# Kernel tuning notes

Hardware: AMD Instinct MI355X
Metric: run time of the kernel (lower is better)

## Reference

```python
import jax, jax.numpy as jnp
import numpy as np

STATE_DIM = 2
HIDDEN = 1024
N_SKILLS = 5
N_ACTIONS = 4
BATCH = 65536


def setup_inputs() -> dict:
    key = jax.random.key(0)
    ks = jax.random.split(key, 8)
    def lin_init(k, fan_in, shape):
        bound = 1.0 / np.sqrt(fan_in)
        return jax.random.uniform(k, shape, jnp.float32, -bound, bound)
    return {
        "s": jax.random.normal(ks[0], (BATCH, STATE_DIM), jnp.float32),
        "skill_idx": jax.random.randint(ks[1], (BATCH,), 0, N_SKILLS, jnp.int32),
        "W1": lin_init(ks[2], STATE_DIM, (STATE_DIM, HIDDEN)),
        "b1": lin_init(ks[3], STATE_DIM, (HIDDEN,)),
        "W2": lin_init(ks[4], HIDDEN, (HIDDEN, HIDDEN)),
        "b2": lin_init(ks[5], HIDDEN, (HIDDEN,)),
        "W_heads": lin_init(ks[6], HIDDEN, (N_SKILLS, HIDDEN, N_ACTIONS)),
        "b_heads": lin_init(ks[7], HIDDEN, (N_SKILLS, N_ACTIONS)),
    }


def reference(s, skill_idx, W1, b1, W2, b2, W_heads, b_heads):
    # shared feature MLP: Linear -> ReLU -> Linear -> ReLU
    h = jax.nn.relu(s @ W1 + b1)            # [B, H]
    feat = jax.nn.relu(h @ W2 + b2)         # [B, H]
    # per-sample skill head: gather weights then one batched contraction
    Wg = W_heads[skill_idx]                 # [B, H, A]
    bg = b_heads[skill_idx]                 # [B, A]
    return jnp.einsum('bh,bha->ba', feat, Wg) + bg  # [B, A]
```

## Files before the change

### kernel.cpp

```cpp
#include <hip/hip_runtime.h>

typedef __bf16 bf16x8 __attribute__((ext_vector_type(8)));
typedef __bf16 bf16x4 __attribute__((ext_vector_type(4)));
typedef float  floatx4 __attribute__((ext_vector_type(4)));

#define GLOBAL_AS __attribute__((address_space(1)))
#define LOCAL_AS  __attribute__((address_space(3)))

static constexpr int HID = 1024;
static constexpr int MT  = 128;
static constexpr int BK  = 64;
static constexpr int KIT = HID / BK;

__device__ __forceinline__ void h8(bf16x8& d, float s0, float s1,
                                   const float4& w0a, const float4& w0b,
                                   const float4& w1a, const float4& w1b,
                                   const float4& ba,  const float4& bb) {
    d[0] = (__bf16)fmaxf(fmaf(s1, w1a.x, fmaf(s0, w0a.x, ba.x)), 0.f);
    d[1] = (__bf16)fmaxf(fmaf(s1, w1a.y, fmaf(s0, w0a.y, ba.y)), 0.f);
    d[2] = (__bf16)fmaxf(fmaf(s1, w1a.z, fmaf(s0, w0a.z, ba.z)), 0.f);
    d[3] = (__bf16)fmaxf(fmaf(s1, w1a.w, fmaf(s0, w0a.w, ba.w)), 0.f);
    d[4] = (__bf16)fmaxf(fmaf(s1, w1b.x, fmaf(s0, w0b.x, bb.x)), 0.f);
    d[5] = (__bf16)fmaxf(fmaf(s1, w1b.y, fmaf(s0, w0b.y, bb.y)), 0.f);
    d[6] = (__bf16)fmaxf(fmaf(s1, w1b.z, fmaf(s0, w0b.z, bb.z)), 0.f);
    d[7] = (__bf16)fmaxf(fmaf(s1, w1b.w, fmaf(s0, w0b.w, bb.w)), 0.f);
}

__global__ __launch_bounds__(256)
void prep_all(const float* __restrict__ S,  const float* __restrict__ W1,
              const float* __restrict__ B1, const float* __restrict__ W2,
              const float* __restrict__ WH,
              __bf16* __restrict__ H, __bf16* __restrict__ W2T,
              __bf16* __restrict__ WHT, float* __restrict__ OUT,
              int row0, int nh, int nz) {
    if (blockIdx.x < (unsigned)nh) {
        const int wid  = blockIdx.x * 4 + (threadIdx.x >> 6);
        const int lane = threadIdx.x & 63;
        const int rb   = wid * 8;
        const int c0   = lane * 8;
        const float4 w0a0 = *(const float4*)(W1 + c0);
        const float4 w0b0 = *(const float4*)(W1 + c0 + 4);
        const float4 w1a0 = *(const float4*)(W1 + HID + c0);
        const float4 w1b0 = *(const float4*)(W1 + HID + c0 + 4);
        const float4 ba0  = *(const float4*)(B1 + c0);
        const float4 bb0  = *(const float4*)(B1 + c0 + 4);
        const float4 w0a1 = *(const float4*)(W1 + 512 + c0);
        const float4 w0b1 = *(const float4*)(W1 + 512 + c0 + 4);
        const float4 w1a1 = *(const float4*)(W1 + HID + 512 + c0);
        const float4 w1b1 = *(const float4*)(W1 + HID + 512 + c0 + 4);
        const float4 ba1  = *(const float4*)(B1 + 512 + c0);
        const float4 bb1  = *(const float4*)(B1 + 512 + c0 + 4);
        float2 sv[8];
#pragma unroll
        for (int r = 0; r < 8; ++r)
            sv[r] = *(const float2*)(S + (size_t)(row0 + rb + r) * 2);
#pragma unroll
        for (int r = 0; r < 8; ++r) {
            const int rl = rb + r;
            const int xo = ((((c0 >> 3) & 7) ^ (rl & 7)) << 3);
            bf16x8 hv0, hv1;
            h8(hv0, sv[r].x, sv[r].y, w0a0, w0b0, w1a0, w1b0, ba0, bb0);
            h8(hv1, sv[r].x, sv[r].y, w0a1, w0b1, w1a1, w1b1, ba1, bb1);
            *(bf16x8*)(H + (size_t)rl * HID + ((c0 & ~63) | xo))       = hv0;
            *(bf16x8*)(H + (size_t)rl * HID + ((c0 & ~63) | xo) + 512) = hv1;
        }
        return;
    }
    int b = blockIdx.x - nh;
    if (b < nz) {
        ((float4*)OUT)[(size_t)row0 + (size_t)b * 256 + threadIdx.x]
            = make_float4(0.f, 0.f, 0.f, 0.f);
        return;
    }
    b -= nz;
    if (b < 256) {
        __shared__ __bf16 tile[64][65];
        const int bx = b & 15;
        const int by = b >> 4;
        const int a  = threadIdx.x & 63;
        const int bb = threadIdx.x >> 6;
#pragma unroll
        for (int r = 0; r < 16; ++r) {
            const int k = r * 4 + bb;
            tile[a][k] = (__bf16)W2[(size_t)(by * 64 + k) * HID + bx * 64 + a];
        }
        __syncthreads();
#pragma unroll
        for (int r = 0; r < 16; ++r) {
            const int n = r * 4 + bb;
            const int g = a >> 3, j = a & 7;
            const int ksw = ((g ^ (n & 7)) << 3) | j;
            W2T[(size_t)(bx * 64 + n) * HID + by * 64 + ksw] = tile[n][a];
        }
    } else {
        const int r = b - 256;
        const int s = r >> 2, a = r & 3;
        for (int k = threadIdx.x; k < HID; k += 256) {
            const float v = (r < 20) ? WH[((size_t)s * HID + k) * 4 + a] : 0.f;
            const int c = k >> 7, o = (k >> 3) & 15, j = k & 7;
            const int sw = (o & 8) | ((o & 7) ^ (r & 7));
            WHT[(size_t)r * HID + c * 128 + sw * 8 + j] = (__bf16)v;
        }
    }
}

__global__ __launch_bounds__(256, 4)
void policy_main(const __bf16* __restrict__ H, const int* __restrict__ SK,
                 const __bf16* __restrict__ W2T, const float* __restrict__ B2,
                 const __bf16* __restrict__ WHT, const float* __restrict__ BH,
                 float* __restrict__ OUT, int row0, int mg_bits) {
    __shared__ __align__(16) char smem[40960];
    __bf16* hA    = (__bf16*)smem;
    __bf16* Bt    = (__bf16*)(smem + 16384);
    __bf16* featL = (__bf16*)smem;
    __bf16* WHTL  = (__bf16*)(smem + 32768);

    const int tid  = threadIdx.x;
    const int lane = tid & 63;
    const int wv   = tid >> 6;
    const int wm   = wv & 1;
    const int wn   = wv >> 1;
    const int l15  = lane & 15;
    const int quad = lane >> 4;
    const int n8   = blockIdx.x >> mg_bits;
    const int i0l  = (blockIdx.x & ((1 << mg_bits) - 1)) * MT;

    floatx4 acc[4][4] = {};
    floatx4 hacc[2][2] = {};

#pragma unroll
    for (int c = 0; c < 2; ++c) {
        const int rb = c * 16 + wv * 4;
        const __bf16* gp = WHT + (size_t)(rb + (lane >> 4)) * HID
                         + n8 * 128 + (lane & 15) * 8;
        __builtin_amdgcn_global_load_lds((GLOBAL_AS void*)gp,
                                         (LOCAL_AS void*)(WHTL + rb * 128), 16, 0, 0);
    }

#pragma unroll 1
    for (int kt = 0; kt < KIT; ++kt) {
        __syncthreads();
#pragma unroll
        for (int c = 0; c < 4; ++c) {
            const int rb = c * 32 + wv * 8;
            const __bf16* gp = H + (size_t)(i0l + rb + (lane >> 3)) * HID
                             + kt * BK + (lane & 7) * 8;
            __builtin_amdgcn_global_load_lds((GLOBAL_AS void*)gp,
                                             (LOCAL_AS void*)(hA + rb * 64), 16, 0, 0);
        }
#pragma unroll
        for (int c = 0; c < 4; ++c) {
            const int rb = c * 32 + wv * 8;
            const __bf16* gp = W2T + (size_t)(n8 * 128 + rb + (lane >> 3)) * HID
                             + kt * BK + (lane & 7) * 8;
            __builtin_amdgcn_global_load_lds((GLOBAL_AS void*)gp,
                                             (LOCAL_AS void*)(Bt + rb * 64), 16, 0, 0);
        }
        __syncthreads();
#pragma unroll
        for (int ks = 0; ks < 2; ++ks) {
            bf16x8 wf[4], hf[4];
#pragma unroll
            for (int f = 0; f < 4; ++f) {
                const int row = wn * 64 + f * 16 + l15;
                wf[f] = *(const bf16x8*)(Bt + row * 64 + (((ks * 4 + quad) ^ (row & 7)) * 8));
            }
#pragma unroll
            for (int f = 0; f < 4; ++f) {
                const int smp = wm * 64 + f * 16 + l15;
                hf[f] = *(const bf16x8*)(hA + smp * 64 + (((ks * 4 + quad) ^ (smp & 7)) * 8));
            }
#pragma unroll
            for (int fn = 0; fn < 4; ++fn)
#pragma unroll
                for (int fm = 0; fm < 4; ++fm)
                    acc[fn][fm] = __builtin_amdgcn_mfma_f32_16x16x32_bf16(
                        wf[fn], hf[fm], acc[fn][fm], 0, 0, 0);
        }
    }

    __syncthreads();
#pragma unroll
    for (int fn = 0; fn < 4; ++fn) {
        const int fcb = wn * 64 + fn * 16 + quad * 4;
        const float4 b2v = *(const float4*)(B2 + n8 * 128 + fcb);
#pragma unroll
        for (int fm = 0; fm < 4; ++fm) {
            const int smp = wm * 64 + fm * 16 + l15;
            const floatx4 v = acc[fn][fm];
            bf16x4 p;
            p[0] = (__bf16)fmaxf(v[0] + b2v.x, 0.f);
            p[1] = (__bf16)fmaxf(v[1] + b2v.y, 0.f);
            p[2] = (__bf16)fmaxf(v[2] + b2v.z, 0.f);
            p[3] = (__bf16)fmaxf(v[3] + b2v.w, 0.f);
            *(bf16x4*)(featL + smp * 128 + (((fcb >> 3) ^ (smp & 15)) << 3) + (fcb & 7)) = p;
        }
    }
    __syncthreads();

#pragma unroll
    for (int f2 = 0; f2 < 2; ++f2) {
#pragma unroll
        for (int ks2 = 0; ks2 < 4; ++ks2) {
            const int row = wv * 32 + f2 * 16 + l15;
            const bf16x8 fa = *(const bf16x8*)(featL + row * 128
                                 + (((ks2 * 4 + quad) ^ (row & 15)) << 3));
#pragma unroll
            for (int t2 = 0; t2 < 2; ++t2) {
                const int r = t2 * 16 + l15;
                const int o = ks2 * 4 + quad;
                const int sw = (o & 8) | ((o & 7) ^ (r & 7));
                const bf16x8 wb = *(const bf16x8*)(WHTL + r * 128 + sw * 8);
                hacc[f2][t2] = __builtin_amdgcn_mfma_f32_16x16x32_bf16(
                    fa, wb, hacc[f2][t2], 0, 0, 0);
            }
        }
    }

#pragma unroll
    for (int f2 = 0; f2 < 2; ++f2)
#pragma unroll
        for (int j = 0; j < 4; ++j) {
            const int smp = wv * 32 + f2 * 16 + quad * 4 + j;
            const int sk  = SK[(size_t)row0 + i0l + smp];
#pragma unroll
            for (int t2 = 0; t2 < 2; ++t2) {
                const int hc = t2 * 16 + l15;
                const int d  = hc - sk * 4;
                if (d >= 0 && d < 4) {
                    float v = hacc[f2][t2][j];
                    if (n8 == 0) v += BH[hc];
                    atomicAdd(&OUT[(size_t)(row0 + i0l + smp) * 4 + d], v);
                }
            }
        }
}

extern "C" void kernel_launch(void* const* d_in, const int* in_sizes, int n_in,
                              void* d_out, int out_size, void* d_ws, size_t ws_size,
                              hipStream_t stream) {
    const float* S  = (const float*)d_in[0];
    const int*   SK = (const int*)d_in[1];
    const float* W1 = (const float*)d_in[2];
    const float* B1 = (const float*)d_in[3];
    const float* W2 = (const float*)d_in[4];
    const float* B2 = (const float*)d_in[5];
    const float* WH = (const float*)d_in[6];
    const float* BH = (const float*)d_in[7];

    char* ws = (char*)d_ws;
    __bf16* W2T = (__bf16*)ws;
    __bf16* WHT = (__bf16*)(ws + 2 * 1024 * 1024);
    __bf16* H   = (__bf16*)(ws + 2 * 1024 * 1024 + 65536);

    const size_t fixed = 2 * 1024 * 1024 + 65536;
    const size_t avail = ws_size > fixed ? ws_size - fixed : 0;
    int nc = 1;
    while (nc < 64 && (size_t)(65536 / nc) * HID * sizeof(__bf16) > avail) nc <<= 1;
    const int Mc = 65536 / nc;
    int mg_bits = 0;
    while ((1 << mg_bits) < Mc / MT) ++mg_bits;

    for (int c = 0; c < nc; ++c) {
        const int nh = Mc / 32;
        const int nz = Mc / 256;
        const int extra = (c == 0) ? 288 : 0;
        hipLaunchKernelGGL(prep_all, dim3(nh + nz + extra), dim3(256), 0, stream,
                           S, W1, B1, W2, WH, H, W2T, WHT, (float*)d_out,
                           c * Mc, nh, nz);
        hipLaunchKernelGGL(policy_main, dim3((Mc / MT) * 8), dim3(256), 0, stream,
                           H, SK, W2T, B2, WHT, BH, (float*)d_out, c * Mc, mg_bits);
    }
}
```

Measured before the change: 239.6 us.

## Fuse prep and GEMM kernels into one persistent cooperative kernel with grid sync

Merges the weight-transpose, hidden-layer computation and output-zeroing kernel with the main GEMM kernel into a single persistent cooperative kernel. A grid-wide barrier separates the two phases, and tiles are processed in a grid-stride loop sized from the occupancy query. This removes one kernel launch per chunk and the gap between the two launches. In exchange it adds grid-sync overhead, and the persistent loop may lose some latency hiding compared with a full oversubscribed grid.

```diff
diff --git a/kernel.cpp b/kernel.cpp
--- a/kernel.cpp
+++ b/kernel.cpp
@@ -1,4 +1,7 @@
 #include <hip/hip_runtime.h>
+#include <hip/hip_cooperative_groups.h>
+
+namespace cg = cooperative_groups;
 
 typedef __bf16 bf16x8 __attribute__((ext_vector_type(8)));
 typedef __bf16 bf16x4 __attribute__((ext_vector_type(4)));
@@ -26,18 +29,59 @@
     d[7] = (__bf16)fmaxf(fmaf(s1, w1b.w, fmaf(s0, w0b.w, bb.w)), 0.f);
 }
 
-__global__ __launch_bounds__(256)
-void prep_all(const float* __restrict__ S,  const float* __restrict__ W1,
-              const float* __restrict__ B1, const float* __restrict__ W2,
-              const float* __restrict__ WH,
-              __bf16* __restrict__ H, __bf16* __restrict__ W2T,
-              __bf16* __restrict__ WHT, float* __restrict__ OUT,
-              int row0, int nh, int nz) {
-    if (blockIdx.x < (unsigned)nh) {
-        const int wid  = blockIdx.x * 4 + (threadIdx.x >> 6);
-        const int lane = threadIdx.x & 63;
-        const int rb   = wid * 8;
-        const int c0   = lane * 8;
+__global__ __launch_bounds__(256, 4)
+void policy_mega(const float* __restrict__ S,  const int* __restrict__ SK,
+                 const float* __restrict__ W1, const float* __restrict__ B1,
+                 const float* __restrict__ W2, const float* __restrict__ B2,
+                 const float* __restrict__ WH, const float* __restrict__ BH,
+                 __bf16* __restrict__ H, __bf16* __restrict__ W2T,
+                 __bf16* __restrict__ WHT, float* __restrict__ OUT,
+                 int row0, int Mc, int mg_bits, int do_weights) {
+    __shared__ __align__(16) char smem[40960];
+    __bf16* hA    = (__bf16*)smem;
+    __bf16* Bt    = (__bf16*)(smem + 16384);
+    __bf16* featL = (__bf16*)smem;
+    __bf16* WHTL  = (__bf16*)(smem + 32768);
+
+    const int tid  = threadIdx.x;
+    const int lane = tid & 63;
+    const int wv   = tid >> 6;
+    const int l15  = lane & 15;
+    const int quad = lane >> 4;
+
+    if (do_weights) {
+        for (int wb = blockIdx.x; wb < 288; wb += gridDim.x) {
+            if (wb < 256) {
+                __bf16 (*tile)[65] = (__bf16 (*)[65])smem;
+                const int bx = wb & 15, by = wb >> 4;
+                const int a = tid & 63, b4 = tid >> 6;
+#pragma unroll
+                for (int r = 0; r < 16; ++r) {
+                    const int k = r * 4 + b4;
+                    tile[a][k] = (__bf16)W2[(size_t)(by * 64 + k) * HID + bx * 64 + a];
+                }
+                __syncthreads();
+#pragma unroll
+                for (int r = 0; r < 16; ++r) {
+                    const int n = r * 4 + b4;
+                    const int g = a >> 3, j = a & 7;
+                    W2T[(size_t)(bx * 64 + n) * HID + by * 64
+                        + (((g ^ (n & 7)) << 3) | j)] = tile[n][a];
+                }
+                __syncthreads();
+            } else {
+                const int r = wb - 256, s = r >> 2, ac = r & 3;
+                for (int k = tid; k < HID; k += 256) {
+                    const float v = (r < 20) ? WH[((size_t)s * HID + k) * 4 + ac] : 0.f;
+                    const int cc = k >> 7, o = (k >> 3) & 15, j = k & 7;
+                    WHT[(size_t)r * HID + cc * 128
+                        + ((o & 8) | ((o & 7) ^ (r & 7))) * 8 + j] = (__bf16)v;
+                }
+            }
+        }
+    }
+    {
+        const int c0 = lane * 8;
         const float4 w0a0 = *(const float4*)(W1 + c0);
         const float4 w0b0 = *(const float4*)(W1 + c0 + 4);
         const float4 w1a0 = *(const float4*)(W1 + HID + c0);
@@ -50,190 +94,156 @@
         const float4 w1b1 = *(const float4*)(W1 + HID + 512 + c0 + 4);
         const float4 ba1  = *(const float4*)(B1 + 512 + c0);
         const float4 bb1  = *(const float4*)(B1 + 512 + c0 + 4);
-        float2 sv[8];
-#pragma unroll
-        for (int r = 0; r < 8; ++r)
-            sv[r] = *(const float2*)(S + (size_t)(row0 + rb + r) * 2);
-#pragma unroll
-        for (int r = 0; r < 8; ++r) {
-            const int rl = rb + r;
-            const int xo = ((((c0 >> 3) & 7) ^ (rl & 7)) << 3);
-            bf16x8 hv0, hv1;
-            h8(hv0, sv[r].x, sv[r].y, w0a0, w0b0, w1a0, w1b0, ba0, bb0);
-            h8(hv1, sv[r].x, sv[r].y, w0a1, w0b1, w1a1, w1b1, ba1, bb1);
-            *(bf16x8*)(H + (size_t)rl * HID + ((c0 & ~63) | xo))       = hv0;
-            *(bf16x8*)(H + (size_t)rl * HID + ((c0 & ~63) | xo) + 512) = hv1;
-        }
-        return;
-    }
-    int b = blockIdx.x - nh;
-    if (b < nz) {
-        ((float4*)OUT)[(size_t)row0 + (size_t)b * 256 + threadIdx.x]
-            = make_float4(0.f, 0.f, 0.f, 0.f);
-        return;
-    }
-    b -= nz;
-    if (b < 256) {
-        __shared__ __bf16 tile[64][65];
-        const int bx = b & 15;
-        const int by = b >> 4;
-        const int a  = threadIdx.x & 63;
-        const int bb = threadIdx.x >> 6;
-#pragma unroll
-        for (int r = 0; r < 16; ++r) {
-            const int k = r * 4 + bb;
-            tile[a][k] = (__bf16)W2[(size_t)(by * 64 + k) * HID + bx * 64 + a];
-        }
+        const int nwav = gridDim.x * 4;
+#pragma unroll 1
+        for (int g = blockIdx.x * 4 + wv; g < (Mc >> 3); g += nwav) {
+            const int rb = g * 8;
+            float2 sv[8];
+#pragma unroll
+            for (int r = 0; r < 8; ++r)
+                sv[r] = *(const float2*)(S + (size_t)(row0 + rb + r) * 2);
+#pragma unroll
+            for (int r = 0; r < 8; ++r) {
+                const int rl = rb + r;
+                const int xo = ((((c0 >> 3) & 7) ^ (rl & 7)) << 3);
+                bf16x8 hv0, hv1;
+                h8(hv0, sv[r].x, sv[r].y, w0a0, w0b0, w1a0, w1b0, ba0, bb0);
+                h8(hv1, sv[r].x, sv[r].y, w0a1, w0b1, w1a1, w1b1, ba1, bb1);
+                *(bf16x8*)(H + (size_t)rl * HID + ((c0 & ~63) | xo))       = hv0;
+                *(bf16x8*)(H + (size_t)rl * HID + ((c0 & ~63) | xo) + 512) = hv1;
+            }
+        }
+    }
+    {
+        const int stride = gridDim.x * 256;
+        for (int i = blockIdx.x * 256 + tid; i < Mc; i += stride)
+            ((float4*)OUT)[(size_t)row0 + i] = make_float4(0.f, 0.f, 0.f, 0.f);
+    }
+
+    cg::this_grid().sync();
+
+    const int ntiles = (Mc / MT) * 8;
+#pragma unroll 1
+    for (int tt = blockIdx.x; tt < ntiles; tt += gridDim.x) {
+        const int n8  = tt >> mg_bits;
+        const int i0l = (tt & ((1 << mg_bits) - 1)) * MT;
+        const int wm  = wv & 1;
+        const int wn  = wv >> 1;
+
         __syncthreads();
 #pragma unroll
-        for (int r = 0; r < 16; ++r) {
-            const int n = r * 4 + bb;
-            const int g = a >> 3, j = a & 7;
-            const int ksw = ((g ^ (n & 7)) << 3) | j;
-            W2T[(size_t)(bx * 64 + n) * HID + by * 64 + ksw] = tile[n][a];
-        }
-    } else {
-        const int r = b - 256;
-        const int s = r >> 2, a = r & 3;
-        for (int k = threadIdx.x; k < HID; k += 256) {
-            const float v = (r < 20) ? WH[((size_t)s * HID + k) * 4 + a] : 0.f;
-            const int c = k >> 7, o = (k >> 3) & 15, j = k & 7;
-            const int sw = (o & 8) | ((o & 7) ^ (r & 7));
-            WHT[(size_t)r * HID + c * 128 + sw * 8 + j] = (__bf16)v;
-        }
-    }
-}
-
-__global__ __launch_bounds__(256, 4)
-void policy_main(const __bf16* __restrict__ H, const int* __restrict__ SK,
-                 const __bf16* __restrict__ W2T, const float* __restrict__ B2,
-                 const __bf16* __restrict__ WHT, const float* __restrict__ BH,
-                 float* __restrict__ OUT, int row0, int mg_bits) {
-    __shared__ __align__(16) char smem[40960];
-    __bf16* hA    = (__bf16*)smem;
-    __bf16* Bt    = (__bf16*)(smem + 16384);
-    __bf16* featL = (__bf16*)smem;
-    __bf16* WHTL  = (__bf16*)(smem + 32768);
-
-    const int tid  = threadIdx.x;
-    const int lane = tid & 63;
-    const int wv   = tid >> 6;
-    const int wm   = wv & 1;
-    const int wn   = wv >> 1;
-    const int l15  = lane & 15;
-    const int quad = lane >> 4;
-    const int n8   = blockIdx.x >> mg_bits;
-    const int i0l  = (blockIdx.x & ((1 << mg_bits) - 1)) * MT;
-
-    floatx4 acc[4][4] = {};
-    floatx4 hacc[2][2] = {};
-
-#pragma unroll
-    for (int c = 0; c < 2; ++c) {
-        const int rb = c * 16 + wv * 4;
-        const __bf16* gp = WHT + (size_t)(rb + (lane >> 4)) * HID
-                         + n8 * 128 + (lane & 15) * 8;
-        __builtin_amdgcn_global_load_lds((GLOBAL_AS void*)gp,
-                                         (LOCAL_AS void*)(WHTL + rb * 128), 16, 0, 0);
-    }
+        for (int c = 0; c < 2; ++c) {
+            const int rb = c * 16 + wv * 4;
+            const __bf16* gp = WHT + (size_t)(rb + (lane >> 4)) * HID
+                             + n8 * 128 + (lane & 15) * 8;
+            __builtin_amdgcn_global_load_lds((GLOBAL_AS void*)gp,
+                                             (LOCAL_AS void*)(WHTL + rb * 128), 16, 0, 0);
+        }
+
+        floatx4 acc[4][4] = {};
+        floatx4 hacc[2][2] = {};
 
 #pragma unroll 1
-    for (int kt = 0; kt < KIT; ++kt) {
+        for (int kt = 0; kt < KIT; ++kt) {
+            __syncthreads();
+#pragma unroll
+            for (int c = 0; c < 4; ++c) {
+                const int rb = c * 32 + wv * 8;
+                const __bf16* gp = H + (size_t)(i0l + rb + (lane >> 3)) * HID
+                                 + kt * BK + (lane & 7) * 8;
+                __builtin_amdgcn_global_load_lds((GLOBAL_AS void*)gp,
+                                                 (LOCAL_AS void*)(hA + rb * 64), 16, 0, 0);
+            }
+#pragma unroll
+            for (int c = 0; c < 4; ++c) {
+                const int rb = c * 32 + wv * 8;
+                const __bf16* gp = W2T + (size_t)(n8 * 128 + rb + (lane >> 3)) * HID
+                                 + kt * BK + (lane & 7) * 8;
+                __builtin_amdgcn_global_load_lds((GLOBAL_AS void*)gp,
+                                                 (LOCAL_AS void*)(Bt + rb * 64), 16, 0, 0);
+            }
+            __syncthreads();
+#pragma unroll
+            for (int ks = 0; ks < 2; ++ks) {
+                bf16x8 wf[4], hf[4];
+#pragma unroll
+                for (int f = 0; f < 4; ++f) {
+                    const int row = wn * 64 + f * 16 + l15;
+                    wf[f] = *(const bf16x8*)(Bt + row * 64
+                                             + (((ks * 4 + quad) ^ (row & 7)) * 8));
+                }
+#pragma unroll
+                for (int f = 0; f < 4; ++f) {
+                    const int smp = wm * 64 + f * 16 + l15;
+                    hf[f] = *(const bf16x8*)(hA + smp * 64
+                                             + (((ks * 4 + quad) ^ (smp & 7)) * 8));
+                }
+#pragma unroll
+                for (int fn = 0; fn < 4; ++fn)
+#pragma unroll
+                    for (int fm = 0; fm < 4; ++fm)
+                        acc[fn][fm] = __builtin_amdgcn_mfma_f32_16x16x32_bf16(
+                            wf[fn], hf[fm], acc[fn][fm], 0, 0, 0);
+            }
+        }
+
         __syncthreads();
 #pragma unroll
-        for (int c = 0; c < 4; ++c) {
-            const int rb = c * 32 + wv * 8;
-            const __bf16* gp = H + (size_t)(i0l + rb + (lane >> 3)) * HID
-                             + kt * BK + (lane & 7) * 8;
-            __builtin_amdgcn_global_load_lds((GLOBAL_AS void*)gp,
-                                             (LOCAL_AS void*)(hA + rb * 64), 16, 0, 0);
-        }
-#pragma unroll
-        for (int c = 0; c < 4; ++c) {
-            const int rb = c * 32 + wv * 8;
-            const __bf16* gp = W2T + (size_t)(n8 * 128 + rb + (lane >> 3)) * HID
-                             + kt * BK + (lane & 7) * 8;
-            __builtin_amdgcn_global_load_lds((GLOBAL_AS void*)gp,
-                                             (LOCAL_AS void*)(Bt + rb * 64), 16, 0, 0);
+        for (int fn = 0; fn < 4; ++fn) {
+            const int fcb = wn * 64 + fn * 16 + quad * 4;
+            const float4 b2v = *(const float4*)(B2 + n8 * 128 + fcb);
+#pragma unroll
+            for (int fm = 0; fm < 4; ++fm) {
+                const int smp = wm * 64 + fm * 16 + l15;
+                const floatx4 v = acc[fn][fm];
+                bf16x4 p;
+                p[0] = (__bf16)fmaxf(v[0] + b2v.x, 0.f);
+                p[1] = (__bf16)fmaxf(v[1] + b2v.y, 0.f);
+                p[2] = (__bf16)fmaxf(v[2] + b2v.z, 0.f);
+                p[3] = (__bf16)fmaxf(v[3] + b2v.w, 0.f);
+                *(bf16x4*)(featL + smp * 128
+                           + (((fcb >> 3) ^ (smp & 15)) << 3) + (fcb & 7)) = p;
+            }
         }
         __syncthreads();
-#pragma unroll
-        for (int ks = 0; ks < 2; ++ks) {
-            bf16x8 wf[4], hf[4];
-#pragma unroll
-            for (int f = 0; f < 4; ++f) {
-                const int row = wn * 64 + f * 16 + l15;
-                wf[f] = *(const bf16x8*)(Bt + row * 64 + (((ks * 4 + quad) ^ (row & 7)) * 8));
-            }
-#pragma unroll
-            for (int f = 0; f < 4; ++f) {
-                const int smp = wm * 64 + f * 16 + l15;
-                hf[f] = *(const bf16x8*)(hA + smp * 64 + (((ks * 4 + quad) ^ (smp & 7)) * 8));
-            }
-#pragma unroll
-            for (int fn = 0; fn < 4; ++fn)
-#pragma unroll
-                for (int fm = 0; fm < 4; ++fm)
-                    acc[fn][fm] = __builtin_amdgcn_mfma_f32_16x16x32_bf16(
-                        wf[fn], hf[fm], acc[fn][fm], 0, 0, 0);
-        }
-    }
-
-    __syncthreads();
-#pragma unroll
-    for (int fn = 0; fn < 4; ++fn) {
-        const int fcb = wn * 64 + fn * 16 + quad * 4;
-        const float4 b2v = *(const float4*)(B2 + n8 * 128 + fcb);
-#pragma unroll
-        for (int fm = 0; fm < 4; ++fm) {
-            const int smp = wm * 64 + fm * 16 + l15;
-            const floatx4 v = acc[fn][fm];
-            bf16x4 p;
-            p[0] = (__bf16)fmaxf(v[0] + b2v.x, 0.f);
-            p[1] = (__bf16)fmaxf(v[1] + b2v.y, 0.f);
-            p[2] = (__bf16)fmaxf(v[2] + b2v.z, 0.f);
-            p[3] = (__bf16)fmaxf(v[3] + b2v.w, 0.f);
-            *(bf16x4*)(featL + smp * 128 + (((fcb >> 3) ^ (smp & 15)) << 3) + (fcb & 7)) = p;
-        }
-    }
-    __syncthreads();
-
-#pragma unroll
-    for (int f2 = 0; f2 < 2; ++f2) {
-#pragma unroll
-        for (int ks2 = 0; ks2 < 4; ++ks2) {
-            const int row = wv * 32 + f2 * 16 + l15;
-            const bf16x8 fa = *(const bf16x8*)(featL + row * 128
-                                 + (((ks2 * 4 + quad) ^ (row & 15)) << 3));
-#pragma unroll
-            for (int t2 = 0; t2 < 2; ++t2) {
-                const int r = t2 * 16 + l15;
-                const int o = ks2 * 4 + quad;
-                const int sw = (o & 8) | ((o & 7) ^ (r & 7));
-                const bf16x8 wb = *(const bf16x8*)(WHTL + r * 128 + sw * 8);
-                hacc[f2][t2] = __builtin_amdgcn_mfma_f32_16x16x32_bf16(
-                    fa, wb, hacc[f2][t2], 0, 0, 0);
-            }
-        }
-    }
-
-#pragma unroll
-    for (int f2 = 0; f2 < 2; ++f2)
-#pragma unroll
-        for (int j = 0; j < 4; ++j) {
-            const int smp = wv * 32 + f2 * 16 + quad * 4 + j;
-            const int sk  = SK[(size_t)row0 + i0l + smp];
-#pragma unroll
-            for (int t2 = 0; t2 < 2; ++t2) {
-                const int hc = t2 * 16 + l15;
-                const int d  = hc - sk * 4;
-                if (d >= 0 && d < 4) {
-                    float v = hacc[f2][t2][j];
-                    if (n8 == 0) v += BH[hc];
-                    atomicAdd(&OUT[(size_t)(row0 + i0l + smp) * 4 + d], v);
-                }
-            }
-        }
+
+#pragma unroll
+        for (int f2 = 0; f2 < 2; ++f2) {
+#pragma unroll
+            for (int ks2 = 0; ks2 < 4; ++ks2) {
+                const int row = wv * 32 + f2 * 16 + l15;
+                const bf16x8 fa = *(const bf16x8*)(featL + row * 128
+                                     + (((ks2 * 4 + quad) ^ (row & 15)) << 3));
+#pragma unroll
+                for (int t2 = 0; t2 < 2; ++t2) {
+                    const int r = t2 * 16 + l15;
+                    const int o = ks2 * 4 + quad;
+                    const int sw = (o & 8) | ((o & 7) ^ (r & 7));
+                    const bf16x8 wb = *(const bf16x8*)(WHTL + r * 128 + sw * 8);
+                    hacc[f2][t2] = __builtin_amdgcn_mfma_f32_16x16x32_bf16(
+                        fa, wb, hacc[f2][t2], 0, 0, 0);
+                }
+            }
+        }
+
+#pragma unroll
+        for (int f2 = 0; f2 < 2; ++f2)
+#pragma unroll
+            for (int j = 0; j < 4; ++j) {
+                const int smp = wv * 32 + f2 * 16 + quad * 4 + j;
+                const int sk  = SK[(size_t)row0 + i0l + smp];
+#pragma unroll
+                for (int t2 = 0; t2 < 2; ++t2) {
+                    const int hc = t2 * 16 + l15;
+                    const int d  = hc - sk * 4;
+                    if (d >= 0 && d < 4) {
+                        float v = hacc[f2][t2][j];
+                        if (n8 == 0) v += BH[hc];
+                        atomicAdd(&OUT[(size_t)(row0 + i0l + smp) * 4 + d], v);
+                    }
+                }
+            }
+    }
 }
 
 extern "C" void kernel_launch(void* const* d_in, const int* in_sizes, int n_in,
@@ -261,14 +271,24 @@
     int mg_bits = 0;
     while ((1 << mg_bits) < Mc / MT) ++mg_bits;
 
+    int occ = 0;
+    hipOccupancyMaxActiveBlocksPerMultiprocessor(&occ, policy_mega, 256, 0);
+    if (occ < 1) occ = 1;
+    if (occ > 4) occ = 4;
+    int grid = occ * 256;
+    if (grid > 1024) grid = 1024;
+
     for (int c = 0; c < nc; ++c) {
-        const int nh = Mc / 32;
-        const int nz = Mc / 256;
-        const int extra = (c == 0) ? 288 : 0;
-        hipLaunchKernelGGL(prep_all, dim3(nh + nz + extra), dim3(256), 0, stream,
-                           S, W1, B1, W2, WH, H, W2T, WHT, (float*)d_out,
-                           c * Mc, nh, nz);
-        hipLaunchKernelGGL(policy_main, dim3((Mc / MT) * 8), dim3(256), 0, stream,
-                           H, SK, W2T, B2, WHT, BH, (float*)d_out, c * Mc, mg_bits);
+        const float* S_ = S;  const int* SK_ = SK;
+        const float* W1_ = W1; const float* B1_ = B1;
+        const float* W2_ = W2; const float* B2_ = B2;
+        const float* WH_ = WH; const float* BH_ = BH;
+        __bf16* H_ = H; __bf16* W2T_ = W2T; __bf16* WHT_ = WHT;
+        float* OUT_ = (float*)d_out;
+        int row0_ = c * Mc, Mc_ = Mc, mgb_ = mg_bits, dw_ = (c == 0) ? 1 : 0;
+        void* args[] = { &S_, &SK_, &W1_, &B1_, &W2_, &B2_, &WH_, &BH_,
+                         &H_, &W2T_, &WHT_, &OUT_, &row0_, &Mc_, &mgb_, &dw_ };
+        hipLaunchCooperativeKernel((void*)policy_mega, dim3(grid), dim3(256),
+                                   args, 0, stream);
     }
 }
```

Result: slower. 398.4 us (+66.3%).
